# Kernel tuning notes

Measured on AMD Instinct MI355X. Metric: run time of the kernel, lower is better.

The kernel has to match this reference:

```python
import jax, jax.numpy as jnp
import numpy as np

B, N, M, H, NH = 128, 4096, 64, 512, 4
IN, OUT = 256, 256
NH2 = 2 * NH  # read/write heads interleaved: even idx = read, odd idx = write
EPS = 1e-8


def setup_inputs() -> dict:
    key = jax.random.key(0)
    ks = jax.random.split(key, 20)
    nrm = lambda k, shape, s=0.05: (jax.random.normal(k, shape, jnp.float32) * s)
    return {
        'in_data': jax.random.normal(ks[0], (B, IN), jnp.float32),
        'memory': jax.random.normal(ks[1], (B, N, M), jnp.float32) * 0.1,
        'h_prev': jax.random.normal(ks[2], (B, H), jnp.float32),
        'c_prev': jax.random.normal(ks[3], (B, H), jnp.float32),
        'prev_reads': jax.random.normal(ks[4], (NH, B, M), jnp.float32),
        'prev_weights': jax.random.uniform(ks[5], (NH2, B, N), jnp.float32),
        # controller LSTMCell (input = in_data ++ prev_reads)
        'W_ih': nrm(ks[6], (4 * H, IN + NH * M)),
        'b_ih': jnp.zeros((4 * H,), jnp.float32),
        'W_hh': nrm(ks[7], (4 * H, H)),
        'b_hh': jnp.zeros((4 * H,), jnp.float32),
        # output layer over [h ++ reads]
        'W_out': nrm(ks[8], (OUT, H + NH * M)),
        'b_out': jnp.zeros((OUT,), jnp.float32),
        # per-head addressing params, stacked over the 2*NH heads (fed with c-state)
        'Wk': nrm(ks[9], (NH2, M, H)), 'bk': jnp.zeros((NH2, M), jnp.float32),
        'Wbeta': nrm(ks[10], (NH2, H)), 'bbeta': jnp.zeros((NH2,), jnp.float32),
        'Wg': nrm(ks[11], (NH2, H)), 'bg': jnp.zeros((NH2,), jnp.float32),
        'Ws': nrm(ks[12], (NH2, 3, H)), 'bs': jnp.zeros((NH2, 3), jnp.float32),
        'Wgam': nrm(ks[13], (NH2, H)), 'bgam': jnp.zeros((NH2,), jnp.float32),
        'We': nrm(ks[14], (NH2, M, H)), 'be': jnp.zeros((NH2, M), jnp.float32),
        'Wa': nrm(ks[15], (NH2, M, H)), 'ba': jnp.zeros((NH2, M), jnp.float32),
    }


def reference(in_data, memory, h_prev, c_prev, prev_reads, prev_weights,
              W_ih, b_ih, W_hh, b_hh, W_out, b_out,
              Wk, bk, Wbeta, bbeta, Wg, bg, Ws, bs, Wgam, bgam, We, be, Wa, ba):
    bsz = in_data.shape[0]
    # controller LSTM step on [x ++ prev_reads]
    x = jnp.concatenate([in_data, jnp.swapaxes(prev_reads, 0, 1).reshape(bsz, -1)], axis=-1)
    gates = x @ W_ih.T + h_prev @ W_hh.T + b_ih + b_hh
    gi, gf, gg, go = jnp.split(gates, 4, axis=-1)
    c = jax.nn.sigmoid(gf) * c_prev + jax.nn.sigmoid(gi) * jnp.tanh(gg)
    h = jax.nn.sigmoid(go) * jnp.tanh(c)  # |h| < 1, so clamp(-20, 20) is identity

    mem = memory
    reads = []
    for i in range(NH2):  # fixed small loop; even = read head, odd = write head
        keyv = c @ Wk[i].T + bk[i]                                    # [B, M]
        beta = jax.nn.softplus(c @ Wbeta[i] + bbeta[i])[:, None]      # [B, 1]
        g = jax.nn.sigmoid(c @ Wg[i] + bg[i])[:, None]                # [B, 1]
        s = jax.nn.softmax(c @ Ws[i].T + bs[i], axis=-1)              # [B, 3]
        gamma = 1.0 + jax.nn.softplus(c @ Wgam[i] + bgam[i])[:, None]  # [B, 1]
        # content addressing: cosine similarity, sharpened softmax
        sim = jnp.einsum('bnm,bm->bn', mem, keyv)
        sim = sim / (jnp.linalg.norm(mem, axis=-1) * jnp.linalg.norm(keyv, axis=-1, keepdims=True) + EPS)
        wc = jax.nn.softmax(beta * sim, axis=-1)
        # interpolate, circular shift (-1, 0, +1), sharpen
        wg_ = g * wc + (1.0 - g) * prev_weights[i]
        wsft = (s[:, 0:1] * jnp.roll(wg_, -1, axis=1)
                + s[:, 1:2] * wg_
                + s[:, 2:3] * jnp.roll(wg_, 1, axis=1))
        wpow = wsft ** gamma
        w = wpow / (jnp.sum(wpow, axis=1, keepdims=True) + EPS)
        if i % 2 == 0:
            reads.append(jnp.einsum('bn,bnm->bm', w, mem))
        else:
            e = jax.nn.sigmoid(c @ We[i].T + be[i])                   # erase [B, M]
            a = jnp.tanh(c @ Wa[i].T + ba[i])                         # add   [B, M]
            mem = mem * (1.0 - w[:, :, None] * e[:, None, :]) + w[:, :, None] * a[:, None, :]

    out = jax.nn.sigmoid(jnp.concatenate([h] + reads, axis=-1) @ W_out.T + b_out)
    return out
```

## Files before the change

kernel.cpp:

```cpp
#include <hip/hip_runtime.h>
#include <math.h>

#define BSZ 128
#define NN_ 4096
#define MM_ 64
#define HH_ 512
#define EPSF 1e-8f

__device__ __forceinline__ float sigmoidf_(float x) { return 1.0f / (1.0f + expf(-x)); }
__device__ __forceinline__ float softplusf_(float x) { return fmaxf(x, 0.0f) + log1pf(expf(-fabsf(x))); }

__global__ __launch_bounds__(256) void k_gemm_gates(const float* __restrict__ in_data,
                                                    const float* __restrict__ prev_reads,
                                                    const float* __restrict__ h_prev,
                                                    const float* __restrict__ W_ih,
                                                    const float* __restrict__ W_hh,
                                                    float* __restrict__ C) {
    __shared__ float Alds[64 * 129];
    __shared__ float Wlds[64 * 65];
    int t = threadIdx.x;
    int k0 = blockIdx.y * 64;
    int n0 = blockIdx.x * 64;
    for (int i = 0; i < 8; ++i) {
        int f = t + 256 * i;
        int row = f >> 4, kk = (f & 15) * 4;
        int k = k0 + kk;
        float4 v;
        if (k < 256) v = *(const float4*)(in_data + (row << 8) + k);
        else if (k < 512) {
            int q = k - 256;
            v = *(const float4*)(prev_reads + (((q >> 6) * BSZ + row) << 6) + (q & 63));
        } else v = *(const float4*)(h_prev + (row << 9) + (k - 512));
        Alds[(kk + 0) * 129 + row] = v.x;
        Alds[(kk + 1) * 129 + row] = v.y;
        Alds[(kk + 2) * 129 + row] = v.z;
        Alds[(kk + 3) * 129 + row] = v.w;
    }
    for (int i = 0; i < 4; ++i) {
        int f = t + 256 * i;
        int o = f >> 4, kk = (f & 15) * 4;
        int j = n0 + o, k = k0 + kk;
        const float* src = (k < 512) ? (W_ih + (size_t)j * 512 + k)
                                     : (W_hh + (size_t)j * 512 + (k - 512));
        float4 v = *(const float4*)src;
        Wlds[(kk + 0) * 65 + o] = v.x;
        Wlds[(kk + 1) * 65 + o] = v.y;
        Wlds[(kk + 2) * 65 + o] = v.z;
        Wlds[(kk + 3) * 65 + o] = v.w;
    }
    __syncthreads();
    int ob = (t & 15) * 4;
    int bb = (t >> 4) * 8;
    float acc[4][8];
#pragma unroll
    for (int i = 0; i < 4; ++i)
#pragma unroll
        for (int j = 0; j < 8; ++j) acc[i][j] = 0.f;
    for (int kk = 0; kk < 64; ++kk) {
        const float* wp = &Wlds[kk * 65 + ob];
        const float* ap = &Alds[kk * 129 + bb];
        float w0 = wp[0], w1 = wp[1], w2 = wp[2], w3 = wp[3];
#pragma unroll
        for (int j = 0; j < 8; ++j) {
            float av = ap[j];
            acc[0][j] = fmaf(w0, av, acc[0][j]);
            acc[1][j] = fmaf(w1, av, acc[1][j]);
            acc[2][j] = fmaf(w2, av, acc[2][j]);
            acc[3][j] = fmaf(w3, av, acc[3][j]);
        }
    }
#pragma unroll
    for (int i = 0; i < 4; ++i)
#pragma unroll
        for (int j = 0; j < 8; ++j)
            atomicAdd(&C[(size_t)(bb + j) * 2048 + n0 + ob + i], acc[i][j]);
}

__device__ __forceinline__ const float* whead_row_ptr(const float* Wk, const float* Wbeta,
                                                      const float* Wg, const float* Ws,
                                                      const float* Wgam, const float* We,
                                                      const float* Wa, int r) {
    int i = r / 198, q = r - i * 198;
    if (q < 64)  return Wk + (size_t)((i << 6) + q) * 512;
    if (q == 64) return Wbeta + (size_t)i * 512;
    if (q == 65) return Wg + (size_t)i * 512;
    if (q <= 68) return Ws + (size_t)(i * 3 + q - 66) * 512;
    if (q == 69) return Wgam + (size_t)i * 512;
    if (q < 134) return We + (size_t)((i << 6) + q - 70) * 512;
    return Wa + (size_t)((i << 6) + q - 134) * 512;
}

__global__ __launch_bounds__(256) void k_gemm_head(const float* __restrict__ A,
                                                   const float* __restrict__ Wk,
                                                   const float* __restrict__ Wbeta,
                                                   const float* __restrict__ Wg,
                                                   const float* __restrict__ Ws,
                                                   const float* __restrict__ Wgam,
                                                   const float* __restrict__ We,
                                                   const float* __restrict__ Wa,
                                                   float* __restrict__ C) {
    __shared__ float Alds[64 * 129];
    __shared__ float Wlds[64 * 65];
    int t = threadIdx.x;
    int k0 = blockIdx.y * 64;
    int n0 = blockIdx.x * 64;
    for (int i = 0; i < 8; ++i) {
        int f = t + 256 * i;
        int row = f >> 4, kk = (f & 15) * 4;
        float4 v = *(const float4*)(A + (size_t)row * 512 + k0 + kk);
        Alds[(kk + 0) * 129 + row] = v.x;
        Alds[(kk + 1) * 129 + row] = v.y;
        Alds[(kk + 2) * 129 + row] = v.z;
        Alds[(kk + 3) * 129 + row] = v.w;
    }
    for (int i = 0; i < 4; ++i) {
        int f = t + 256 * i;
        int o = f >> 4, kk = (f & 15) * 4;
        int r = n0 + o;
        float4 v = make_float4(0.f, 0.f, 0.f, 0.f);
        if (r < 1386) {
            const float* p = whead_row_ptr(Wk, Wbeta, Wg, Ws, Wgam, We, Wa, r) + k0 + kk;
            v = *(const float4*)p;
        }
        Wlds[(kk + 0) * 65 + o] = v.x;
        Wlds[(kk + 1) * 65 + o] = v.y;
        Wlds[(kk + 2) * 65 + o] = v.z;
        Wlds[(kk + 3) * 65 + o] = v.w;
    }
    __syncthreads();
    int ob = (t & 15) * 4;
    int bb = (t >> 4) * 8;
    float acc[4][8];
#pragma unroll
    for (int i = 0; i < 4; ++i)
#pragma unroll
        for (int j = 0; j < 8; ++j) acc[i][j] = 0.f;
    for (int kk = 0; kk < 64; ++kk) {
        const float* wp = &Wlds[kk * 65 + ob];
        const float* ap = &Alds[kk * 129 + bb];
        float w0 = wp[0], w1 = wp[1], w2 = wp[2], w3 = wp[3];
#pragma unroll
        for (int j = 0; j < 8; ++j) {
            float av = ap[j];
            acc[0][j] = fmaf(w0, av, acc[0][j]);
            acc[1][j] = fmaf(w1, av, acc[1][j]);
            acc[2][j] = fmaf(w2, av, acc[2][j]);
            acc[3][j] = fmaf(w3, av, acc[3][j]);
        }
    }
#pragma unroll
    for (int i = 0; i < 4; ++i)
#pragma unroll
        for (int j = 0; j < 8; ++j)
            atomicAdd(&C[(size_t)(bb + j) * 1408 + n0 + ob + i], acc[i][j]);
}

__global__ __launch_bounds__(256) void k_gemm_out(const float* __restrict__ hbuf,
                                                  const float* __restrict__ rbuf,
                                                  const float* __restrict__ W_out,
                                                  float* __restrict__ C) {
    __shared__ float Alds[64 * 129];
    __shared__ float Wlds[64 * 65];
    int t = threadIdx.x;
    int k0 = blockIdx.y * 64;
    int n0 = blockIdx.x * 64;
    for (int i = 0; i < 8; ++i) {
        int f = t + 256 * i;
        int row = f >> 4, kk = (f & 15) * 4;
        int k = k0 + kk;
        float4 v;
        if (k < 512) v = *(const float4*)(hbuf + (row << 9) + k);
        else {
            int q = k - 512;
            v = *(const float4*)(rbuf + (((q >> 6) * BSZ + row) << 6) + (q & 63));
        }
        Alds[(kk + 0) * 129 + row] = v.x;
        Alds[(kk + 1) * 129 + row] = v.y;
        Alds[(kk + 2) * 129 + row] = v.z;
        Alds[(kk + 3) * 129 + row] = v.w;
    }
    for (int i = 0; i < 4; ++i) {
        int f = t + 256 * i;
        int o = f >> 4, kk = (f & 15) * 4;
        float4 v = *(const float4*)(W_out + (size_t)(n0 + o) * 768 + k0 + kk);
        Wlds[(kk + 0) * 65 + o] = v.x;
        Wlds[(kk + 1) * 65 + o] = v.y;
        Wlds[(kk + 2) * 65 + o] = v.z;
        Wlds[(kk + 3) * 65 + o] = v.w;
    }
    __syncthreads();
    int ob = (t & 15) * 4;
    int bb = (t >> 4) * 8;
    float acc[4][8];
#pragma unroll
    for (int i = 0; i < 4; ++i)
#pragma unroll
        for (int j = 0; j < 8; ++j) acc[i][j] = 0.f;
    for (int kk = 0; kk < 64; ++kk) {
        const float* wp = &Wlds[kk * 65 + ob];
        const float* ap = &Alds[kk * 129 + bb];
        float w0 = wp[0], w1 = wp[1], w2 = wp[2], w3 = wp[3];
#pragma unroll
        for (int j = 0; j < 8; ++j) {
            float av = ap[j];
            acc[0][j] = fmaf(w0, av, acc[0][j]);
            acc[1][j] = fmaf(w1, av, acc[1][j]);
            acc[2][j] = fmaf(w2, av, acc[2][j]);
            acc[3][j] = fmaf(w3, av, acc[3][j]);
        }
    }
#pragma unroll
    for (int i = 0; i < 4; ++i)
#pragma unroll
        for (int j = 0; j < 8; ++j)
            atomicAdd(&C[(size_t)(bb + j) * 256 + n0 + ob + i], acc[i][j]);
}

__global__ void k_lstm(const float* __restrict__ gates, const float* __restrict__ b_ih,
                       const float* __restrict__ b_hh, const float* __restrict__ c_prev,
                       float* __restrict__ cbuf, float* __restrict__ hbuf) {
    int idx = blockIdx.x * blockDim.x + threadIdx.x;
    if (idx >= BSZ * HH_) return;
    int b = idx >> 9, j = idx & 511;
    const float* gr = gates + (size_t)b * 2048;
    float gi = gr[j]        + b_ih[j]        + b_hh[j];
    float gf = gr[512 + j]  + b_ih[512 + j]  + b_hh[512 + j];
    float gg = gr[1024 + j] + b_ih[1024 + j] + b_hh[1024 + j];
    float go = gr[1536 + j] + b_ih[1536 + j] + b_hh[1536 + j];
    float cc = sigmoidf_(gf) * c_prev[idx] + sigmoidf_(gi) * tanhf(gg);
    float hh = sigmoidf_(go) * tanhf(cc);
    cbuf[idx] = cc;
    hbuf[idx] = hh;
}

__global__ __launch_bounds__(256) void k_headact(const float* __restrict__ Chead,
                                                 const float* __restrict__ bk, const float* __restrict__ bbeta,
                                                 const float* __restrict__ bg, const float* __restrict__ bs,
                                                 const float* __restrict__ bgam, const float* __restrict__ be,
                                                 const float* __restrict__ ba,
                                                 float* __restrict__ keys, float* __restrict__ knorm,
                                                 float* __restrict__ betaA, float* __restrict__ gA,
                                                 float* __restrict__ gammaA, float* __restrict__ sA,
                                                 float* __restrict__ eA, float* __restrict__ aA) {
    __shared__ float sk[64];
    __shared__ float s3[3];
    int blk = blockIdx.x;
    int i = blk >> 7, b = blk & 127;
    int q = threadIdx.x;
    float val = 0.f;
    if (q < 198) {
        float bv = (q < 64)   ? bk[(i << 6) + q]
                 : (q == 64)  ? bbeta[i]
                 : (q == 65)  ? bg[i]
                 : (q <= 68)  ? bs[i * 3 + q - 66]
                 : (q == 69)  ? bgam[i]
                 : (q < 134)  ? be[(i << 6) + q - 70]
                              : ba[(i << 6) + q - 134];
        val = Chead[(size_t)b * 1408 + i * 198 + q] + bv;
    }
    if (q < 64) { keys[(size_t)(i * BSZ + b) * 64 + q] = val; sk[q] = val * val; }
    if (q >= 66 && q <= 68) s3[q - 66] = val;
    __syncthreads();
    if (q == 0) {
        float s = 0.f;
        for (int m2 = 0; m2 < 64; ++m2) s += sk[m2];
        knorm[i * BSZ + b] = sqrtf(s);
    }
    if (q == 64) betaA[i * BSZ + b] = softplusf_(val);
    if (q == 65) gA[i * BSZ + b] = sigmoidf_(val);
    if (q == 69) gammaA[i * BSZ + b] = 1.f + softplusf_(val);
    if (q == 66) {
        float mx = fmaxf(s3[0], fmaxf(s3[1], s3[2]));
        float e0 = expf(s3[0] - mx), e1 = expf(s3[1] - mx), e2 = expf(s3[2] - mx);
        float inv = 1.f / (e0 + e1 + e2);
        sA[(i * BSZ + b) * 3 + 0] = e0 * inv;
        sA[(i * BSZ + b) * 3 + 1] = e1 * inv;
        sA[(i * BSZ + b) * 3 + 2] = e2 * inv;
    }
    if (q >= 70 && q < 134)  eA[(size_t)(i * BSZ + b) * 64 + (q - 70)] = sigmoidf_(val);
    if (q >= 134 && q < 198) aA[(size_t)(i * BSZ + b) * 64 + (q - 134)] = tanhf(val);
}

__global__ __launch_bounds__(256) void k_pass2(const float* __restrict__ mem,
                                               const float* __restrict__ wbuf,
                                               const float* __restrict__ eA, const float* __restrict__ aA,
                                               const float* __restrict__ keys, const float* __restrict__ knorm,
                                               float* __restrict__ sims, float* __restrict__ r_out,
                                               int napply, int nsims, int sh0, int sh1,
                                               int read_state, int read_head, int read_idx) {
    __shared__ __align__(16) float rbuf[16][64];
    int t = threadIdx.x;
    int lane = t & 15, grp = t >> 4;
    int base = blockIdx.x * 64;
    int b = base >> 12;
    int m4 = lane * 4;
    float4 e1 = *(const float4*)(eA + (size_t)(1 * BSZ + b) * 64 + m4);
    float4 a1 = *(const float4*)(aA + (size_t)(1 * BSZ + b) * 64 + m4);
    float4 e3 = *(const float4*)(eA + (size_t)(3 * BSZ + b) * 64 + m4);
    float4 a3 = *(const float4*)(aA + (size_t)(3 * BSZ + b) * 64 + m4);
    float4 e5 = *(const float4*)(eA + (size_t)(5 * BSZ + b) * 64 + m4);
    float4 a5 = *(const float4*)(aA + (size_t)(5 * BSZ + b) * 64 + m4);
    float4 k0v = make_float4(0.f, 0.f, 0.f, 0.f), k1v = k0v;
    float kn0v = 0.f, kn1v = 0.f;
    if (nsims > 0) { k0v = *(const float4*)(keys + (size_t)(sh0 * BSZ + b) * 64 + m4); kn0v = knorm[sh0 * BSZ + b]; }
    if (nsims > 1) { k1v = *(const float4*)(keys + (size_t)(sh1 * BSZ + b) * 64 + m4); kn1v = knorm[sh1 * BSZ + b]; }
    const float* w1p = wbuf + (size_t)1 * BSZ * NN_;
    const float* w3p = wbuf + (size_t)3 * BSZ * NN_;
    const float* w5p = wbuf + (size_t)5 * BSZ * NN_;
    const float* wrp = (read_head >= 0) ? (wbuf + (size_t)read_head * BSZ * NN_) : nullptr;
    float* sim0 = sims + (size_t)sh0 * BSZ * NN_;
    float* sim1 = sims + (size_t)sh1 * BSZ * NN_;

    float4 racc = make_float4(0.f, 0.f, 0.f, 0.f);
    for (int it = 0; it < 4; ++it) {
        int row = base + it * 16 + grp;
        float4 m = *(const float4*)(mem + (size_t)row * 64 + m4);
        float4 mr = m;
        if (napply >= 1) {
            float w = w1p[row];
            m.x = m.x * (1.f - w * e1.x) + w * a1.x;
            m.y = m.y * (1.f - w * e1.y) + w * a1.y;
            m.z = m.z * (1.f - w * e1.z) + w * a1.z;
            m.w = m.w * (1.f - w * e1.w) + w * a1.w;
            if (read_state == 1) mr = m;
        }
        if (napply >= 2) {
            float w = w3p[row];
            m.x = m.x * (1.f - w * e3.x) + w * a3.x;
            m.y = m.y * (1.f - w * e3.y) + w * a3.y;
            m.z = m.z * (1.f - w * e3.z) + w * a3.z;
            m.w = m.w * (1.f - w * e3.w) + w * a3.w;
            if (read_state == 2) mr = m;
        }
        if (napply >= 3) {
            float w = w5p[row];
            m.x = m.x * (1.f - w * e5.x) + w * a5.x;
            m.y = m.y * (1.f - w * e5.y) + w * a5.y;
            m.z = m.z * (1.f - w * e5.z) + w * a5.z;
            m.w = m.w * (1.f - w * e5.w) + w * a5.w;
            if (read_state == 3) mr = m;
        }
        if (read_head >= 0) {
            float wr = wrp[row];
            racc.x = fmaf(wr, mr.x, racc.x);
            racc.y = fmaf(wr, mr.y, racc.y);
            racc.z = fmaf(wr, mr.z, racc.z);
            racc.w = fmaf(wr, mr.w, racc.w);
        }
        if (nsims > 0) {
            float d0 = m.x * k0v.x + m.y * k0v.y + m.z * k0v.z + m.w * k0v.w;
            float nn = m.x * m.x + m.y * m.y + m.z * m.z + m.w * m.w;
            float d1 = 0.f;
            if (nsims > 1) d1 = m.x * k1v.x + m.y * k1v.y + m.z * k1v.z + m.w * k1v.w;
#pragma unroll
            for (int off = 8; off >= 1; off >>= 1) {
                d0 += __shfl_xor(d0, off, 16);
                nn += __shfl_xor(nn, off, 16);
                if (nsims > 1) d1 += __shfl_xor(d1, off, 16);
            }
            if (lane == 0) {
                float nm = sqrtf(nn);
                sim0[row] = d0 / (nm * kn0v + EPSF);
                if (nsims > 1) sim1[row] = d1 / (nm * kn1v + EPSF);
            }
        }
    }
    if (read_head >= 0) {
        *(float4*)(&rbuf[grp][m4]) = racc;
        __syncthreads();
        if (t < 64) {
            float s = 0.f;
#pragma unroll
            for (int g2 = 0; g2 < 16; ++g2) s += rbuf[g2][t];
            atomicAdd(&r_out[(size_t)(read_idx * BSZ + b) * 64 + t], s);
        }
    }
}

__global__ __launch_bounds__(1024) void k_weights(const float* __restrict__ sims,
                                                  const float* __restrict__ prev_w,
                                                  const float* __restrict__ betaA, const float* __restrict__ gA,
                                                  const float* __restrict__ gammaA, const float* __restrict__ sA,
                                                  float* __restrict__ wout_base, int head0) {
    __shared__ float wg[NN_];
    __shared__ float redm[16], reds[16], redp[16];
    int h = head0 + blockIdx.y, b = blockIdx.x;
    int hb = h * BSZ + b;
    float beta = betaA[hb], g = gA[hb], gamma = gammaA[hb];
    float s0 = sA[hb * 3 + 0], s1 = sA[hb * 3 + 1], s2 = sA[hb * 3 + 2];
    const float* sim = sims + (size_t)hb * NN_;
    const float* pw = prev_w + (size_t)hb * NN_;
    float* wout = wout_base + (size_t)hb * NN_;
    int t = threadIdx.x, wv = t >> 6, ln = t & 63;
    float tv[4];
    float lmax = -3.4e38f;
#pragma unroll
    for (int j = 0; j < 4; ++j) {
        float x = beta * sim[t + 1024 * j];
        tv[j] = x;
        lmax = fmaxf(lmax, x);
    }
#pragma unroll
    for (int off = 32; off >= 1; off >>= 1) lmax = fmaxf(lmax, __shfl_xor(lmax, off));
    if (ln == 0) redm[wv] = lmax;
    __syncthreads();
    float Mx = redm[0];
#pragma unroll
    for (int k = 1; k < 16; ++k) Mx = fmaxf(Mx, redm[k]);
    float lsum = 0.f;
#pragma unroll
    for (int j = 0; j < 4; ++j) { float ex = expf(tv[j] - Mx); tv[j] = ex; lsum += ex; }
#pragma unroll
    for (int off = 32; off >= 1; off >>= 1) lsum += __shfl_xor(lsum, off);
    if (ln == 0) reds[wv] = lsum;
    __syncthreads();
    float S = 0.f;
#pragma unroll
    for (int k = 0; k < 16; ++k) S += reds[k];
    float invS = 1.f / S;
#pragma unroll
    for (int j = 0; j < 4; ++j) {
        int n = t + 1024 * j;
        wg[n] = g * tv[j] * invS + (1.f - g) * pw[n];
    }
    __syncthreads();
    float lsum2 = 0.f;
#pragma unroll
    for (int j = 0; j < 4; ++j) {
        int n = t + 1024 * j;
        float wsft = s0 * wg[(n + 1) & (NN_ - 1)] + s1 * wg[n] + s2 * wg[(n - 1) & (NN_ - 1)];
        float wp = powf(wsft, gamma);
        tv[j] = wp;
        lsum2 += wp;
    }
#pragma unroll
    for (int off = 32; off >= 1; off >>= 1) lsum2 += __shfl_xor(lsum2, off);
    if (ln == 0) redp[wv] = lsum2;
    __syncthreads();
    float S2 = 0.f;
#pragma unroll
    for (int k = 0; k < 16; ++k) S2 += redp[k];
    float inv2 = 1.f / (S2 + EPSF);
#pragma unroll
    for (int j = 0; j < 4; ++j) wout[t + 1024 * j] = tv[j] * inv2;
}

__global__ void k_out(const float* __restrict__ outacc, const float* __restrict__ b_out,
                      float* __restrict__ out) {
    int idx = blockIdx.x * blockDim.x + threadIdx.x;
    if (idx >= BSZ * 256) return;
    out[idx] = sigmoidf_(outacc[idx] + b_out[idx & 255]);
}

extern "C" void kernel_launch(void* const* d_in, const int* in_sizes, int n_in,
                              void* d_out, int out_size, void* d_ws, size_t ws_size,
                              hipStream_t stream) {
    const float* in_data      = (const float*)d_in[0];
    const float* memory       = (const float*)d_in[1];
    const float* h_prev       = (const float*)d_in[2];
    const float* c_prev       = (const float*)d_in[3];
    const float* prev_reads   = (const float*)d_in[4];
    const float* prev_weights = (const float*)d_in[5];
    const float* W_ih = (const float*)d_in[6];
    const float* b_ih = (const float*)d_in[7];
    const float* W_hh = (const float*)d_in[8];
    const float* b_hh = (const float*)d_in[9];
    const float* W_out = (const float*)d_in[10];
    const float* b_out = (const float*)d_in[11];
    const float* Wk   = (const float*)d_in[12];
    const float* bk   = (const float*)d_in[13];
    const float* Wbeta = (const float*)d_in[14];
    const float* bbeta = (const float*)d_in[15];
    const float* Wg   = (const float*)d_in[16];
    const float* bg   = (const float*)d_in[17];
    const float* Ws   = (const float*)d_in[18];
    const float* bs   = (const float*)d_in[19];
    const float* Wgam = (const float*)d_in[20];
    const float* bgam = (const float*)d_in[21];
    const float* We   = (const float*)d_in[22];
    const float* be   = (const float*)d_in[23];
    const float* Wa   = (const float*)d_in[24];
    const float* ba   = (const float*)d_in[25];

    float* ws = (float*)d_ws;
    size_t o_gates  = 0;
    size_t o_chead  = o_gates + 262144;
    size_t o_r      = o_chead + 180224;
    size_t o_outacc = o_r + 32768;
    size_t zero_floats = o_outacc + 32768;
    size_t o_c     = zero_floats;
    size_t o_h     = o_c + 65536;
    size_t o_keys  = o_h + 65536;
    size_t o_knorm = o_keys + 57344;
    size_t o_beta  = o_knorm + 1024;
    size_t o_g     = o_beta + 1024;
    size_t o_gamma = o_g + 1024;
    size_t o_s     = o_gamma + 1024;
    size_t o_e     = o_s + 3072;
    size_t o_a     = o_e + 57344;
    size_t o_sims  = o_a + 57344;
    size_t o_w     = o_sims + 3670016;

    float* gates  = ws + o_gates;
    float* Chead  = ws + o_chead;
    float* rbuf   = ws + o_r;
    float* outacc = ws + o_outacc;
    float* cbuf   = ws + o_c;
    float* hbuf   = ws + o_h;
    float* keys   = ws + o_keys;
    float* knorm  = ws + o_knorm;
    float* betaA  = ws + o_beta;
    float* gA     = ws + o_g;
    float* gammaA = ws + o_gamma;
    float* sA     = ws + o_s;
    float* eA     = ws + o_e;
    float* aA     = ws + o_a;
    float* sims   = ws + o_sims;
    float* wbuf   = ws + o_w;

    hipMemsetAsync(d_ws, 0, zero_floats * sizeof(float), stream);

    k_gemm_gates<<<dim3(32, 16), 256, 0, stream>>>(in_data, prev_reads, h_prev, W_ih, W_hh, gates);
    k_lstm<<<256, 256, 0, stream>>>(gates, b_ih, b_hh, c_prev, cbuf, hbuf);

    k_gemm_head<<<dim3(22, 8), 256, 0, stream>>>(cbuf, Wk, Wbeta, Wg, Ws, Wgam, We, Wa, Chead);
    k_headact<<<896, 256, 0, stream>>>(Chead, bk, bbeta, bg, bs, bgam, be, ba,
                                       keys, knorm, betaA, gA, gammaA, sA, eA, aA);

    const int PB = BSZ * NN_ / 64;
    k_pass2<<<PB, 256, 0, stream>>>(memory, wbuf, eA, aA, keys, knorm, sims, rbuf,
                                    0, 2, 0, 1, -1, -1, 0);
    k_weights<<<dim3(128, 2), 1024, 0, stream>>>(sims, prev_weights, betaA, gA, gammaA, sA, wbuf, 0);
    k_pass2<<<PB, 256, 0, stream>>>(memory, wbuf, eA, aA, keys, knorm, sims, rbuf,
                                    1, 2, 2, 3, 0, 0, 0);
    k_weights<<<dim3(128, 2), 1024, 0, stream>>>(sims, prev_weights, betaA, gA, gammaA, sA, wbuf, 2);
    k_pass2<<<PB, 256, 0, stream>>>(memory, wbuf, eA, aA, keys, knorm, sims, rbuf,
                                    2, 2, 4, 5, 1, 2, 1);
    k_weights<<<dim3(128, 2), 1024, 0, stream>>>(sims, prev_weights, betaA, gA, gammaA, sA, wbuf, 4);
    k_pass2<<<PB, 256, 0, stream>>>(memory, wbuf, eA, aA, keys, knorm, sims, rbuf,
                                    3, 1, 6, 6, 2, 4, 2);
    k_weights<<<dim3(128, 1), 1024, 0, stream>>>(sims, prev_weights, betaA, gA, gammaA, sA, wbuf, 6);
    k_pass2<<<PB, 256, 0, stream>>>(memory, wbuf, eA, aA, keys, knorm, sims, rbuf,
                                    3, 0, 0, 0, 3, 6, 3);

    k_gemm_out<<<dim3(4, 12), 256, 0, stream>>>(hbuf, rbuf, W_out, outacc);
    k_out<<<128, 256, 0, stream>>>(outacc, b_out, (float*)d_out);

    (void)in_sizes; (void)n_in; (void)out_size; (void)ws_size;
}
```

Baseline: 534.7 us.

## Fuse memory sweeps and weight passes into one cooperative persistent kernel

Replaces the nine alternating sweep and weight-normalisation launches with a single cooperative kernel that uses grid-wide syncs between phases. Each phase loops over its work with a grid-stride loop, and the weights phase now uses 256-thread blocks instead of 1024. The output GEMM and sigmoid are merged into one non-atomic kernel that no longer needs an accumulator buffer or a separate activation launch. This is meant to remove launch gaps and atomics, at the risk of lower occupancy for the bandwidth-bound sweeps and the cost of the grid barriers. The output GEMM also runs on only 8 blocks.

```diff
diff --git a/kernel.cpp b/kernel.cpp
--- a/kernel.cpp
+++ b/kernel.cpp
@@ -1,5 +1,8 @@
 #include <hip/hip_runtime.h>
+#include <hip/hip_cooperative_groups.h>
 #include <math.h>
+
+namespace cg = cooperative_groups;
 
 #define BSZ 128
 #define NN_ 4096
@@ -155,67 +158,6 @@
             atomicAdd(&C[(size_t)(bb + j) * 1408 + n0 + ob + i], acc[i][j]);
 }
 
-__global__ __launch_bounds__(256) void k_gemm_out(const float* __restrict__ hbuf,
-                                                  const float* __restrict__ rbuf,
-                                                  const float* __restrict__ W_out,
-                                                  float* __restrict__ C) {
-    __shared__ float Alds[64 * 129];
-    __shared__ float Wlds[64 * 65];
-    int t = threadIdx.x;
-    int k0 = blockIdx.y * 64;
-    int n0 = blockIdx.x * 64;
-    for (int i = 0; i < 8; ++i) {
-        int f = t + 256 * i;
-        int row = f >> 4, kk = (f & 15) * 4;
-        int k = k0 + kk;
-        float4 v;
-        if (k < 512) v = *(const float4*)(hbuf + (row << 9) + k);
-        else {
-            int q = k - 512;
-            v = *(const float4*)(rbuf + (((q >> 6) * BSZ + row) << 6) + (q & 63));
-        }
-        Alds[(kk + 0) * 129 + row] = v.x;
-        Alds[(kk + 1) * 129 + row] = v.y;
-        Alds[(kk + 2) * 129 + row] = v.z;
-        Alds[(kk + 3) * 129 + row] = v.w;
-    }
-    for (int i = 0; i < 4; ++i) {
-        int f = t + 256 * i;
-        int o = f >> 4, kk = (f & 15) * 4;
-        float4 v = *(const float4*)(W_out + (size_t)(n0 + o) * 768 + k0 + kk);
-        Wlds[(kk + 0) * 65 + o] = v.x;
-        Wlds[(kk + 1) * 65 + o] = v.y;
-        Wlds[(kk + 2) * 65 + o] = v.z;
-        Wlds[(kk + 3) * 65 + o] = v.w;
-    }
-    __syncthreads();
-    int ob = (t & 15) * 4;
-    int bb = (t >> 4) * 8;
-    float acc[4][8];
-#pragma unroll
-    for (int i = 0; i < 4; ++i)
-#pragma unroll
-        for (int j = 0; j < 8; ++j) acc[i][j] = 0.f;
-    for (int kk = 0; kk < 64; ++kk) {
-        const float* wp = &Wlds[kk * 65 + ob];
-        const float* ap = &Alds[kk * 129 + bb];
-        float w0 = wp[0], w1 = wp[1], w2 = wp[2], w3 = wp[3];
-#pragma unroll
-        for (int j = 0; j < 8; ++j) {
-            float av = ap[j];
-            acc[0][j] = fmaf(w0, av, acc[0][j]);
-            acc[1][j] = fmaf(w1, av, acc[1][j]);
-            acc[2][j] = fmaf(w2, av, acc[2][j]);
-            acc[3][j] = fmaf(w3, av, acc[3][j]);
-        }
-    }
-#pragma unroll
-    for (int i = 0; i < 4; ++i)
-#pragma unroll
-        for (int j = 0; j < 8; ++j)
-            atomicAdd(&C[(size_t)(bb + j) * 256 + n0 + ob + i], acc[i][j]);
-}
-
 __global__ void k_lstm(const float* __restrict__ gates, const float* __restrict__ b_ih,
                        const float* __restrict__ b_hh, const float* __restrict__ c_prev,
                        float* __restrict__ cbuf, float* __restrict__ hbuf) {
@@ -281,175 +223,262 @@
     if (q >= 134 && q < 198) aA[(size_t)(i * BSZ + b) * 64 + (q - 134)] = tanhf(val);
 }
 
-__global__ __launch_bounds__(256) void k_pass2(const float* __restrict__ mem,
-                                               const float* __restrict__ wbuf,
-                                               const float* __restrict__ eA, const float* __restrict__ aA,
-                                               const float* __restrict__ keys, const float* __restrict__ knorm,
-                                               float* __restrict__ sims, float* __restrict__ r_out,
-                                               int napply, int nsims, int sh0, int sh1,
-                                               int read_state, int read_head, int read_idx) {
-    __shared__ __align__(16) float rbuf[16][64];
+__device__ __forceinline__ void dev_sweep(const float* __restrict__ mem,
+                                          const float* __restrict__ wbuf,
+                                          const float* __restrict__ eA, const float* __restrict__ aA,
+                                          const float* __restrict__ keys, const float* __restrict__ knorm,
+                                          float* __restrict__ sims, float* __restrict__ r_out,
+                                          float* smem,
+                                          int napply, int nsims, int sh0, int sh1,
+                                          int read_state, int read_head, int read_idx) {
     int t = threadIdx.x;
     int lane = t & 15, grp = t >> 4;
-    int base = blockIdx.x * 64;
-    int b = base >> 12;
     int m4 = lane * 4;
-    float4 e1 = *(const float4*)(eA + (size_t)(1 * BSZ + b) * 64 + m4);
-    float4 a1 = *(const float4*)(aA + (size_t)(1 * BSZ + b) * 64 + m4);
-    float4 e3 = *(const float4*)(eA + (size_t)(3 * BSZ + b) * 64 + m4);
-    float4 a3 = *(const float4*)(aA + (size_t)(3 * BSZ + b) * 64 + m4);
-    float4 e5 = *(const float4*)(eA + (size_t)(5 * BSZ + b) * 64 + m4);
-    float4 a5 = *(const float4*)(aA + (size_t)(5 * BSZ + b) * 64 + m4);
-    float4 k0v = make_float4(0.f, 0.f, 0.f, 0.f), k1v = k0v;
-    float kn0v = 0.f, kn1v = 0.f;
-    if (nsims > 0) { k0v = *(const float4*)(keys + (size_t)(sh0 * BSZ + b) * 64 + m4); kn0v = knorm[sh0 * BSZ + b]; }
-    if (nsims > 1) { k1v = *(const float4*)(keys + (size_t)(sh1 * BSZ + b) * 64 + m4); kn1v = knorm[sh1 * BSZ + b]; }
     const float* w1p = wbuf + (size_t)1 * BSZ * NN_;
     const float* w3p = wbuf + (size_t)3 * BSZ * NN_;
     const float* w5p = wbuf + (size_t)5 * BSZ * NN_;
     const float* wrp = (read_head >= 0) ? (wbuf + (size_t)read_head * BSZ * NN_) : nullptr;
     float* sim0 = sims + (size_t)sh0 * BSZ * NN_;
     float* sim1 = sims + (size_t)sh1 * BSZ * NN_;
-
-    float4 racc = make_float4(0.f, 0.f, 0.f, 0.f);
-    for (int it = 0; it < 4; ++it) {
-        int row = base + it * 16 + grp;
-        float4 m = *(const float4*)(mem + (size_t)row * 64 + m4);
-        float4 mr = m;
-        if (napply >= 1) {
-            float w = w1p[row];
-            m.x = m.x * (1.f - w * e1.x) + w * a1.x;
-            m.y = m.y * (1.f - w * e1.y) + w * a1.y;
-            m.z = m.z * (1.f - w * e1.z) + w * a1.z;
-            m.w = m.w * (1.f - w * e1.w) + w * a1.w;
-            if (read_state == 1) mr = m;
-        }
-        if (napply >= 2) {
-            float w = w3p[row];
-            m.x = m.x * (1.f - w * e3.x) + w * a3.x;
-            m.y = m.y * (1.f - w * e3.y) + w * a3.y;
-            m.z = m.z * (1.f - w * e3.z) + w * a3.z;
-            m.w = m.w * (1.f - w * e3.w) + w * a3.w;
-            if (read_state == 2) mr = m;
-        }
-        if (napply >= 3) {
-            float w = w5p[row];
-            m.x = m.x * (1.f - w * e5.x) + w * a5.x;
-            m.y = m.y * (1.f - w * e5.y) + w * a5.y;
-            m.z = m.z * (1.f - w * e5.z) + w * a5.z;
-            m.w = m.w * (1.f - w * e5.w) + w * a5.w;
-            if (read_state == 3) mr = m;
+    const int NVB = BSZ * NN_ / 64;
+    for (int vb = blockIdx.x; vb < NVB; vb += gridDim.x) {
+        int base = vb * 64;
+        int b = base >> 12;
+        float4 e1 = *(const float4*)(eA + (size_t)(1 * BSZ + b) * 64 + m4);
+        float4 a1 = *(const float4*)(aA + (size_t)(1 * BSZ + b) * 64 + m4);
+        float4 e3 = *(const float4*)(eA + (size_t)(3 * BSZ + b) * 64 + m4);
+        float4 a3 = *(const float4*)(aA + (size_t)(3 * BSZ + b) * 64 + m4);
+        float4 e5 = *(const float4*)(eA + (size_t)(5 * BSZ + b) * 64 + m4);
+        float4 a5 = *(const float4*)(aA + (size_t)(5 * BSZ + b) * 64 + m4);
+        float4 k0v = make_float4(0.f, 0.f, 0.f, 0.f), k1v = k0v;
+        float kn0v = 0.f, kn1v = 0.f;
+        if (nsims > 0) { k0v = *(const float4*)(keys + (size_t)(sh0 * BSZ + b) * 64 + m4); kn0v = knorm[sh0 * BSZ + b]; }
+        if (nsims > 1) { k1v = *(const float4*)(keys + (size_t)(sh1 * BSZ + b) * 64 + m4); kn1v = knorm[sh1 * BSZ + b]; }
+        float4 racc = make_float4(0.f, 0.f, 0.f, 0.f);
+        for (int it = 0; it < 4; ++it) {
+            int row = base + it * 16 + grp;
+            float4 m = *(const float4*)(mem + (size_t)row * 64 + m4);
+            float4 mr = m;
+            if (napply >= 1) {
+                float w = w1p[row];
+                m.x = m.x * (1.f - w * e1.x) + w * a1.x;
+                m.y = m.y * (1.f - w * e1.y) + w * a1.y;
+                m.z = m.z * (1.f - w * e1.z) + w * a1.z;
+                m.w = m.w * (1.f - w * e1.w) + w * a1.w;
+                if (read_state == 1) mr = m;
+            }
+            if (napply >= 2) {
+                float w = w3p[row];
+                m.x = m.x * (1.f - w * e3.x) + w * a3.x;
+                m.y = m.y * (1.f - w * e3.y) + w * a3.y;
+                m.z = m.z * (1.f - w * e3.z) + w * a3.z;
+                m.w = m.w * (1.f - w * e3.w) + w * a3.w;
+                if (read_state == 2) mr = m;
+            }
+            if (napply >= 3) {
+                float w = w5p[row];
+                m.x = m.x * (1.f - w * e5.x) + w * a5.x;
+                m.y = m.y * (1.f - w * e5.y) + w * a5.y;
+                m.z = m.z * (1.f - w * e5.z) + w * a5.z;
+                m.w = m.w * (1.f - w * e5.w) + w * a5.w;
+                if (read_state == 3) mr = m;
+            }
+            if (read_head >= 0) {
+                float wr = wrp[row];
+                racc.x = fmaf(wr, mr.x, racc.x);
+                racc.y = fmaf(wr, mr.y, racc.y);
+                racc.z = fmaf(wr, mr.z, racc.z);
+                racc.w = fmaf(wr, mr.w, racc.w);
+            }
+            if (nsims > 0) {
+                float d0 = m.x * k0v.x + m.y * k0v.y + m.z * k0v.z + m.w * k0v.w;
+                float nn = m.x * m.x + m.y * m.y + m.z * m.z + m.w * m.w;
+                float d1 = 0.f;
+                if (nsims > 1) d1 = m.x * k1v.x + m.y * k1v.y + m.z * k1v.z + m.w * k1v.w;
+#pragma unroll
+                for (int off = 8; off >= 1; off >>= 1) {
+                    d0 += __shfl_xor(d0, off, 16);
+                    nn += __shfl_xor(nn, off, 16);
+                    if (nsims > 1) d1 += __shfl_xor(d1, off, 16);
+                }
+                if (lane == 0) {
+                    float nm = sqrtf(nn);
+                    sim0[row] = d0 / (nm * kn0v + EPSF);
+                    if (nsims > 1) sim1[row] = d1 / (nm * kn1v + EPSF);
+                }
+            }
         }
         if (read_head >= 0) {
-            float wr = wrp[row];
-            racc.x = fmaf(wr, mr.x, racc.x);
-            racc.y = fmaf(wr, mr.y, racc.y);
-            racc.z = fmaf(wr, mr.z, racc.z);
-            racc.w = fmaf(wr, mr.w, racc.w);
-        }
-        if (nsims > 0) {
-            float d0 = m.x * k0v.x + m.y * k0v.y + m.z * k0v.z + m.w * k0v.w;
-            float nn = m.x * m.x + m.y * m.y + m.z * m.z + m.w * m.w;
-            float d1 = 0.f;
-            if (nsims > 1) d1 = m.x * k1v.x + m.y * k1v.y + m.z * k1v.z + m.w * k1v.w;
-#pragma unroll
-            for (int off = 8; off >= 1; off >>= 1) {
-                d0 += __shfl_xor(d0, off, 16);
-                nn += __shfl_xor(nn, off, 16);
-                if (nsims > 1) d1 += __shfl_xor(d1, off, 16);
-            }
-            if (lane == 0) {
-                float nm = sqrtf(nn);
-                sim0[row] = d0 / (nm * kn0v + EPSF);
-                if (nsims > 1) sim1[row] = d1 / (nm * kn1v + EPSF);
-            }
-        }
-    }
-    if (read_head >= 0) {
-        *(float4*)(&rbuf[grp][m4]) = racc;
-        __syncthreads();
-        if (t < 64) {
-            float s = 0.f;
-#pragma unroll
-            for (int g2 = 0; g2 < 16; ++g2) s += rbuf[g2][t];
-            atomicAdd(&r_out[(size_t)(read_idx * BSZ + b) * 64 + t], s);
-        }
-    }
-}
-
-__global__ __launch_bounds__(1024) void k_weights(const float* __restrict__ sims,
-                                                  const float* __restrict__ prev_w,
-                                                  const float* __restrict__ betaA, const float* __restrict__ gA,
-                                                  const float* __restrict__ gammaA, const float* __restrict__ sA,
-                                                  float* __restrict__ wout_base, int head0) {
-    __shared__ float wg[NN_];
-    __shared__ float redm[16], reds[16], redp[16];
-    int h = head0 + blockIdx.y, b = blockIdx.x;
-    int hb = h * BSZ + b;
-    float beta = betaA[hb], g = gA[hb], gamma = gammaA[hb];
-    float s0 = sA[hb * 3 + 0], s1 = sA[hb * 3 + 1], s2 = sA[hb * 3 + 2];
-    const float* sim = sims + (size_t)hb * NN_;
-    const float* pw = prev_w + (size_t)hb * NN_;
-    float* wout = wout_base + (size_t)hb * NN_;
+            *(float4*)(&smem[grp * 64 + m4]) = racc;
+            __syncthreads();
+            if (t < 64) {
+                float s = 0.f;
+#pragma unroll
+                for (int g2 = 0; g2 < 16; ++g2) s += smem[g2 * 64 + t];
+                atomicAdd(&r_out[(size_t)(read_idx * BSZ + b) * 64 + t], s);
+            }
+            __syncthreads();
+        }
+    }
+}
+
+__device__ __forceinline__ void dev_weights(const float* __restrict__ sims,
+                                            const float* __restrict__ prev_w,
+                                            const float* __restrict__ betaA, const float* __restrict__ gA,
+                                            const float* __restrict__ gammaA, const float* __restrict__ sA,
+                                            float* __restrict__ wout_base, float* smem,
+                                            int head0, int nheads) {
+    float* wg = smem;
+    float* red = smem + 4096;
     int t = threadIdx.x, wv = t >> 6, ln = t & 63;
-    float tv[4];
-    float lmax = -3.4e38f;
-#pragma unroll
-    for (int j = 0; j < 4; ++j) {
-        float x = beta * sim[t + 1024 * j];
-        tv[j] = x;
-        lmax = fmaxf(lmax, x);
-    }
-#pragma unroll
-    for (int off = 32; off >= 1; off >>= 1) lmax = fmaxf(lmax, __shfl_xor(lmax, off));
-    if (ln == 0) redm[wv] = lmax;
-    __syncthreads();
-    float Mx = redm[0];
-#pragma unroll
-    for (int k = 1; k < 16; ++k) Mx = fmaxf(Mx, redm[k]);
-    float lsum = 0.f;
-#pragma unroll
-    for (int j = 0; j < 4; ++j) { float ex = expf(tv[j] - Mx); tv[j] = ex; lsum += ex; }
-#pragma unroll
-    for (int off = 32; off >= 1; off >>= 1) lsum += __shfl_xor(lsum, off);
-    if (ln == 0) reds[wv] = lsum;
-    __syncthreads();
-    float S = 0.f;
-#pragma unroll
-    for (int k = 0; k < 16; ++k) S += reds[k];
-    float invS = 1.f / S;
-#pragma unroll
-    for (int j = 0; j < 4; ++j) {
-        int n = t + 1024 * j;
-        wg[n] = g * tv[j] * invS + (1.f - g) * pw[n];
-    }
-    __syncthreads();
-    float lsum2 = 0.f;
-#pragma unroll
-    for (int j = 0; j < 4; ++j) {
-        int n = t + 1024 * j;
-        float wsft = s0 * wg[(n + 1) & (NN_ - 1)] + s1 * wg[n] + s2 * wg[(n - 1) & (NN_ - 1)];
-        float wp = powf(wsft, gamma);
-        tv[j] = wp;
-        lsum2 += wp;
-    }
-#pragma unroll
-    for (int off = 32; off >= 1; off >>= 1) lsum2 += __shfl_xor(lsum2, off);
-    if (ln == 0) redp[wv] = lsum2;
-    __syncthreads();
-    float S2 = 0.f;
-#pragma unroll
-    for (int k = 0; k < 16; ++k) S2 += redp[k];
-    float inv2 = 1.f / (S2 + EPSF);
-#pragma unroll
-    for (int j = 0; j < 4; ++j) wout[t + 1024 * j] = tv[j] * inv2;
-}
-
-__global__ void k_out(const float* __restrict__ outacc, const float* __restrict__ b_out,
-                      float* __restrict__ out) {
-    int idx = blockIdx.x * blockDim.x + threadIdx.x;
-    if (idx >= BSZ * 256) return;
-    out[idx] = sigmoidf_(outacc[idx] + b_out[idx & 255]);
+    int npairs = nheads * BSZ;
+    for (int p = blockIdx.x; p < npairs; p += gridDim.x) {
+        int h = head0 + (p >> 7), b = p & 127;
+        int hb = h * BSZ + b;
+        float beta = betaA[hb], g = gA[hb], gamma = gammaA[hb];
+        float s0 = sA[hb * 3 + 0], s1 = sA[hb * 3 + 1], s2 = sA[hb * 3 + 2];
+        const float* sim = sims + (size_t)hb * NN_;
+        const float* pw = prev_w + (size_t)hb * NN_;
+        float* wout = wout_base + (size_t)hb * NN_;
+        float tv[16];
+        float lmax = -3.4e38f;
+#pragma unroll
+        for (int j = 0; j < 16; ++j) {
+            float x = beta * sim[t + 256 * j];
+            tv[j] = x;
+            lmax = fmaxf(lmax, x);
+        }
+#pragma unroll
+        for (int off = 32; off >= 1; off >>= 1) lmax = fmaxf(lmax, __shfl_xor(lmax, off));
+        if (ln == 0) red[wv] = lmax;
+        __syncthreads();
+        float Mx = fmaxf(fmaxf(red[0], red[1]), fmaxf(red[2], red[3]));
+        float lsum = 0.f;
+#pragma unroll
+        for (int j = 0; j < 16; ++j) { float ex = expf(tv[j] - Mx); tv[j] = ex; lsum += ex; }
+#pragma unroll
+        for (int off = 32; off >= 1; off >>= 1) lsum += __shfl_xor(lsum, off);
+        if (ln == 0) red[4 + wv] = lsum;
+        __syncthreads();
+        float invS = 1.f / (red[4] + red[5] + red[6] + red[7]);
+#pragma unroll
+        for (int j = 0; j < 16; ++j) {
+            int n = t + 256 * j;
+            wg[n] = g * tv[j] * invS + (1.f - g) * pw[n];
+        }
+        __syncthreads();
+        float lsum2 = 0.f;
+#pragma unroll
+        for (int j = 0; j < 16; ++j) {
+            int n = t + 256 * j;
+            float wsft = s0 * wg[(n + 1) & (NN_ - 1)] + s1 * wg[n] + s2 * wg[(n - 1) & (NN_ - 1)];
+            float wp = powf(wsft, gamma);
+            tv[j] = wp;
+            lsum2 += wp;
+        }
+#pragma unroll
+        for (int off = 32; off >= 1; off >>= 1) lsum2 += __shfl_xor(lsum2, off);
+        if (ln == 0) red[8 + wv] = lsum2;
+        __syncthreads();
+        float inv2 = 1.f / (red[8] + red[9] + red[10] + red[11] + EPSF);
+#pragma unroll
+        for (int j = 0; j < 16; ++j) wout[t + 256 * j] = tv[j] * inv2;
+        __syncthreads();
+    }
+}
+
+__global__ __launch_bounds__(256) void k_mega(const float* __restrict__ mem,
+                                              float* __restrict__ wbuf,
+                                              const float* __restrict__ eA, const float* __restrict__ aA,
+                                              const float* __restrict__ keys, const float* __restrict__ knorm,
+                                              float* __restrict__ sims, float* __restrict__ r_out,
+                                              const float* __restrict__ prev_w,
+                                              const float* __restrict__ betaA, const float* __restrict__ gA,
+                                              const float* __restrict__ gammaA, const float* __restrict__ sA) {
+    cg::grid_group grid = cg::this_grid();
+    __shared__ float smem[4096 + 16];
+    dev_sweep(mem, wbuf, eA, aA, keys, knorm, sims, r_out, smem, 0, 2, 0, 1, -1, -1, 0);
+    grid.sync();
+    dev_weights(sims, prev_w, betaA, gA, gammaA, sA, wbuf, smem, 0, 2);
+    grid.sync();
+    dev_sweep(mem, wbuf, eA, aA, keys, knorm, sims, r_out, smem, 1, 2, 2, 3, 0, 0, 0);
+    grid.sync();
+    dev_weights(sims, prev_w, betaA, gA, gammaA, sA, wbuf, smem, 2, 2);
+    grid.sync();
+    dev_sweep(mem, wbuf, eA, aA, keys, knorm, sims, r_out, smem, 2, 2, 4, 5, 1, 2, 1);
+    grid.sync();
+    dev_weights(sims, prev_w, betaA, gA, gammaA, sA, wbuf, smem, 4, 2);
+    grid.sync();
+    dev_sweep(mem, wbuf, eA, aA, keys, knorm, sims, r_out, smem, 3, 1, 6, 6, 2, 4, 2);
+    grid.sync();
+    dev_weights(sims, prev_w, betaA, gA, gammaA, sA, wbuf, smem, 6, 1);
+    grid.sync();
+    dev_sweep(mem, wbuf, eA, aA, keys, knorm, sims, r_out, smem, 3, 0, 0, 0, 3, 6, 3);
+}
+
+__global__ __launch_bounds__(256) void k_out_full(const float* __restrict__ hbuf,
+                                                  const float* __restrict__ rbuf,
+                                                  const float* __restrict__ W_out,
+                                                  const float* __restrict__ b_out,
+                                                  float* __restrict__ out) {
+    __shared__ float Alds[64 * 65];
+    __shared__ float Wlds[64 * 65];
+    int t = threadIdx.x;
+    int n0 = blockIdx.x * 64;
+    int b0 = blockIdx.y * 64;
+    int ob = (t & 15) * 4;
+    int bb = (t >> 4) * 4;
+    float acc[4][4];
+#pragma unroll
+    for (int i = 0; i < 4; ++i)
+#pragma unroll
+        for (int j = 0; j < 4; ++j) acc[i][j] = 0.f;
+    for (int k0 = 0; k0 < 768; k0 += 64) {
+        __syncthreads();
+        for (int i = 0; i < 4; ++i) {
+            int f = t + 256 * i;
+            int rb = f >> 4, kk = (f & 15) * 4;
+            int k = k0 + kk;
+            float4 v;
+            if (k < 512) v = *(const float4*)(hbuf + ((b0 + rb) << 9) + k);
+            else {
+                int q = k - 512;
+                v = *(const float4*)(rbuf + (((q >> 6) * BSZ + b0 + rb) << 6) + (q & 63));
+            }
+            Alds[(kk + 0) * 65 + rb] = v.x;
+            Alds[(kk + 1) * 65 + rb] = v.y;
+            Alds[(kk + 2) * 65 + rb] = v.z;
+            Alds[(kk + 3) * 65 + rb] = v.w;
+        }
+        for (int i = 0; i < 4; ++i) {
+            int f = t + 256 * i;
+            int o = f >> 4, kk = (f & 15) * 4;
+            float4 v = *(const float4*)(W_out + (size_t)(n0 + o) * 768 + k0 + kk);
+            Wlds[(kk + 0) * 65 + o] = v.x;
+            Wlds[(kk + 1) * 65 + o] = v.y;
+            Wlds[(kk + 2) * 65 + o] = v.z;
+            Wlds[(kk + 3) * 65 + o] = v.w;
+        }
+        __syncthreads();
+        for (int kk = 0; kk < 64; ++kk) {
+            const float* wp = &Wlds[kk * 65 + ob];
+            const float* ap = &Alds[kk * 65 + bb];
+            float w0 = wp[0], w1 = wp[1], w2 = wp[2], w3 = wp[3];
+#pragma unroll
+            for (int j = 0; j < 4; ++j) {
+                float av = ap[j];
+                acc[0][j] = fmaf(w0, av, acc[0][j]);
+                acc[1][j] = fmaf(w1, av, acc[1][j]);
+                acc[2][j] = fmaf(w2, av, acc[2][j]);
+                acc[3][j] = fmaf(w3, av, acc[3][j]);
+            }
+        }
+    }
+#pragma unroll
+    for (int i = 0; i < 4; ++i)
+#pragma unroll
+        for (int j = 0; j < 4; ++j)
+            out[(size_t)(b0 + bb + j) * 256 + n0 + ob + i] = sigmoidf_(acc[i][j] + b_out[n0 + ob + i]);
 }
 
 extern "C" void kernel_launch(void* const* d_in, const int* in_sizes, int n_in,
@@ -486,8 +515,7 @@
     size_t o_gates  = 0;
     size_t o_chead  = o_gates + 262144;
     size_t o_r      = o_chead + 180224;
-    size_t o_outacc = o_r + 32768;
-    size_t zero_floats = o_outacc + 32768;
+    size_t zero_floats = o_r + 32768;
     size_t o_c     = zero_floats;
     size_t o_h     = o_c + 65536;
     size_t o_keys  = o_h + 65536;
@@ -504,7 +532,6 @@
     float* gates  = ws + o_gates;
     float* Chead  = ws + o_chead;
     float* rbuf   = ws + o_r;
-    float* outacc = ws + o_outacc;
     float* cbuf   = ws + o_c;
     float* hbuf   = ws + o_h;
     float* keys   = ws + o_keys;
@@ -518,6 +545,20 @@
     float* sims   = ws + o_sims;
     float* wbuf   = ws + o_w;
 
+    static int g_grid = 0;
+    if (g_grid == 0) {
+        int dev = 0;
+        hipGetDevice(&dev);
+        int ncu = 0;
+        hipDeviceGetAttribute(&ncu, hipDeviceAttributeMultiprocessorCount, dev);
+        int maxb = 0;
+        hipOccupancyMaxActiveBlocksPerMultiprocessor(&maxb, k_mega, 256, 0);
+        if (ncu <= 0) ncu = 256;
+        if (maxb <= 0) maxb = 1;
+        g_grid = ncu * maxb;
+        if (g_grid > 8192) g_grid = 8192;
+    }
+
     hipMemsetAsync(d_ws, 0, zero_floats * sizeof(float), stream);
 
     k_gemm_gates<<<dim3(32, 16), 256, 0, stream>>>(in_data, prev_reads, h_prev, W_ih, W_hh, gates);
@@ -527,24 +568,17 @@
     k_headact<<<896, 256, 0, stream>>>(Chead, bk, bbeta, bg, bs, bgam, be, ba,
                                        keys, knorm, betaA, gA, gammaA, sA, eA, aA);
 
-    const int PB = BSZ * NN_ / 64;
-    k_pass2<<<PB, 256, 0, stream>>>(memory, wbuf, eA, aA, keys, knorm, sims, rbuf,
-                                    0, 2, 0, 1, -1, -1, 0);
-    k_weights<<<dim3(128, 2), 1024, 0, stream>>>(sims, prev_weights, betaA, gA, gammaA, sA, wbuf, 0);
-    k_pass2<<<PB, 256, 0, stream>>>(memory, wbuf, eA, aA, keys, knorm, sims, rbuf,
-                                    1, 2, 2, 3, 0, 0, 0);
-    k_weights<<<dim3(128, 2), 1024, 0, stream>>>(sims, prev_weights, betaA, gA, gammaA, sA, wbuf, 2);
-    k_pass2<<<PB, 256, 0, stream>>>(memory, wbuf, eA, aA, keys, knorm, sims, rbuf,
-                                    2, 2, 4, 5, 1, 2, 1);
-    k_weights<<<dim3(128, 2), 1024, 0, stream>>>(sims, prev_weights, betaA, gA, gammaA, sA, wbuf, 4);
-    k_pass2<<<PB, 256, 0, stream>>>(memory, wbuf, eA, aA, keys, knorm, sims, rbuf,
-                                    3, 1, 6, 6, 2, 4, 2);
-    k_weights<<<dim3(128, 1), 1024, 0, stream>>>(sims, prev_weights, betaA, gA, gammaA, sA, wbuf, 6);
-    k_pass2<<<PB, 256, 0, stream>>>(memory, wbuf, eA, aA, keys, knorm, sims, rbuf,
-                                    3, 0, 0, 0, 3, 6, 3);
-
-    k_gemm_out<<<dim3(4, 12), 256, 0, stream>>>(hbuf, rbuf, W_out, outacc);
-    k_out<<<128, 256, 0, stream>>>(outacc, b_out, (float*)d_out);
+    {
+        void* margs[] = {
+            (void*)&memory, (void*)&wbuf, (void*)&eA, (void*)&aA, (void*)&keys,
+            (void*)&knorm, (void*)&sims, (void*)&rbuf, (void*)&prev_weights,
+            (void*)&betaA, (void*)&gA, (void*)&gammaA, (void*)&sA
+        };
+        hipLaunchCooperativeKernel((const void*)k_mega, dim3(g_grid), dim3(256),
+                                   (void**)margs, 0, stream);
+    }
+
+    k_out_full<<<dim3(4, 2), 256, 0, stream>>>(hbuf, rbuf, W_out, b_out, (float*)d_out);
 
     (void)in_sizes; (void)n_in; (void)out_size; (void)ws_size;
 }
```

Measured after the change: 1.123 ms. 110% more time.
